# Optimization experiments

Measured on AMD Instinct MI355X. Metric: run time of the kernel, lower is better.

## Reference

```python
import jax, jax.numpy as jnp
import numpy as np

N = 4096        # number_of_users
IN = 1000       # in_size (items)
H1, H2 = 2048, 1024
EMB = 512
HEADS = 8
OUT = 1000


def setup_inputs() -> dict:
    key = jax.random.key(0)
    ks = iter(jax.random.split(key, 32))
    def lin(i, o):
        return jax.random.normal(next(ks), (i, o), jnp.float32) * (1.0 / np.sqrt(i))
    inp = {"batch": jax.random.normal(next(ks), (N, IN), jnp.float32)}
    for p in ("q", "k", "v"):
        inp[p + "_w1"] = lin(IN, H1); inp[p + "_b1"] = jnp.zeros((H1,), jnp.float32)
        inp[p + "_w2"] = lin(H1, H2); inp[p + "_b2"] = jnp.zeros((H2,), jnp.float32)
        inp[p + "_w3"] = lin(H2, EMB); inp[p + "_b3"] = jnp.zeros((EMB,), jnp.float32)
    inp["wo_w"] = lin(EMB, OUT)
    inp["wo_b"] = jnp.zeros((OUT,), jnp.float32)
    return inp


def _mlp(x, w1, b1, w2, b2, w3, b3):
    h = jax.nn.relu(x @ w1 + b1)
    h = jax.nn.relu(h @ w2 + b2)
    return h @ w3 + b3


def _split_heads(x):
    # [N, EMB] -> [HEADS, N, depth]
    return x.reshape(N, HEADS, EMB // HEADS).transpose(1, 0, 2)


def reference(batch,
              q_w1, q_b1, q_w2, q_b2, q_w3, q_b3,
              k_w1, k_b1, k_w2, k_b2, k_w3, k_b3,
              v_w1, v_b1, v_w2, v_b2, v_w3, v_b3,
              wo_w, wo_b):
    q = _mlp(batch, q_w1, q_b1, q_w2, q_b2, q_w3, q_b3)
    k = _mlp(batch, k_w1, k_b1, k_w2, k_b2, k_w3, k_b3)
    v = _mlp(batch, v_w1, v_b1, v_w2, v_b2, v_w3, v_b3)
    qh = jax.nn.relu(_split_heads(q))
    kh = jax.nn.relu(_split_heads(k))
    vh = _split_heads(v)
    depth = EMB // HEADS
    # ReLU-normalized attention (no softmax): scores / row-sum
    scores = jnp.einsum('hnd,hmd->hnm', qh, kh) / jnp.sqrt(jnp.float32(depth))
    denom = jnp.sum(scores, axis=-1, keepdims=True) + 1e-8
    weights = scores / denom
    att = jnp.einsum('hnm,hmd->hnd', weights, vh)   # [H, N, depth]
    att = att.transpose(1, 0, 2).reshape(N, EMB)
    return att @ wo_w + wo_b
```

## Files before the change

### kernel.cpp

```cpp
#include <hip/hip_runtime.h>
#include <hip/hip_bf16.h>


typedef __attribute__((ext_vector_type(4))) float f32x4;
typedef __attribute__((ext_vector_type(8))) short bf16x8;

static constexpr size_t OFF_XB   = 0;
static constexpr size_t OFF_WT1  = OFF_XB   + 8388608;
static constexpr size_t OFF_WT2  = OFF_WT1  + 12582912;
static constexpr size_t OFF_WT3  = OFF_WT2  + 12582912;
static constexpr size_t OFF_WTO  = OFF_WT3  + 3145728;
static constexpr size_t OFF_B1C  = OFF_WTO  + 1048576;
static constexpr size_t OFF_H1   = OFF_B1C  + 24576;
static constexpr size_t OFF_H2   = OFF_H1   + 50331648;
static constexpr size_t OFF_QKV  = OFF_H2   + 25165824;
static constexpr size_t OFF_MP   = OFF_QKV  + 12582912;
static constexpr size_t OFF_MF   = OFF_MP   + 4259840;
static constexpr size_t OFF_ATT  = OFF_MF   + 133120;

__device__ __forceinline__ void gload16(const __hip_bfloat16* g, __hip_bfloat16* l) {
  __builtin_amdgcn_global_load_lds(
      (const __attribute__((address_space(1))) void*)g,
      (__attribute__((address_space(3))) void*)l, 16, 0, 0);
}

__global__ void conv_pad_batch(const float* __restrict__ in, __hip_bfloat16* __restrict__ out) {
  int idx = blockIdx.x * 256 + threadIdx.x;
  int r = idx >> 10, c = idx & 1023;
  float v = (c < 1000) ? in[(size_t)r * 1000 + c] : 0.f;
  out[idx] = __float2bfloat16(v);
}

__global__ void concat3(const float* __restrict__ a, const float* __restrict__ b,
                        const float* __restrict__ c, float* __restrict__ out) {
  int i = blockIdx.x * 256 + threadIdx.x;
  if (i < 6144) {
    const float* src = (i < 2048) ? a : ((i < 4096) ? b : c);
    out[i] = src[i & 2047];
  }
}

__global__ void transpose_conv3(const float* __restrict__ s0, const float* __restrict__ s1,
                                const float* __restrict__ s2, __hip_bfloat16* __restrict__ outb,
                                size_t ostride, int K, int N, int Kpad) {
  const float* in = (blockIdx.z == 0) ? s0 : ((blockIdx.z == 1) ? s1 : s2);
  __hip_bfloat16* out = outb + (size_t)blockIdx.z * ostride;
  __shared__ float tile[32][33];
  int kb = blockIdx.x * 32, nb = blockIdx.y * 32;
  int tx = threadIdx.x, ty = threadIdx.y;
  for (int i = ty; i < 32; i += 8) {
    int k = kb + i, n = nb + tx;
    tile[i][tx] = (k < K && n < N) ? in[(size_t)k * N + n] : 0.f;
  }
  __syncthreads();
  for (int i = ty; i < 32; i += 8) {
    int n = nb + i, kp = kb + tx;
    out[(size_t)n * Kpad + kp] = __float2bfloat16(tile[tx][i]);
  }
}

__global__ __launch_bounds__(512, 2) void gemm_p8(
    const __hip_bfloat16* __restrict__ A, int lda, size_t Az,
    const __hip_bfloat16* __restrict__ B, int ldb, size_t Bz,
    const float* __restrict__ bias0, const float* __restrict__ bias1,
    const float* __restrict__ bias2,
    __hip_bfloat16* __restrict__ Cout, int ldc, size_t Cz,
    int NT, int relu) {
  __shared__ __hip_bfloat16 sm[2][4][8192];
  const int t = threadIdx.x;
  const int z = blockIdx.z;
  const int m0 = blockIdx.y * 256, n0 = blockIdx.x * 256;
  A += (size_t)z * Az;
  B += (size_t)z * Bz;
  const float* bias = (z == 0) ? bias0 : ((z == 1) ? bias1 : bias2);

  const int w = t >> 6, l = t & 63;
  const int wm = w >> 2, wn = w & 3;
  const int fr = l & 15, fq = l >> 4;

  const int row0 = t >> 3, row1 = row0 + 64;
  const int c0 = (t & 7) ^ (row0 & 7);
  const int c1 = (t & 7) ^ (row1 & 7);
  const __hip_bfloat16* gA0a = A + (size_t)(m0 + row0) * lda + c0 * 8;
  const __hip_bfloat16* gA0b = A + (size_t)(m0 + row1) * lda + c1 * 8;
  const __hip_bfloat16* gA1a = gA0a + (size_t)128 * lda;
  const __hip_bfloat16* gA1b = gA0b + (size_t)128 * lda;
  const __hip_bfloat16* gB0a = B + (size_t)(n0 + row0) * ldb + c0 * 8;
  const __hip_bfloat16* gB0b = B + (size_t)(n0 + row1) * ldb + c1 * 8;
  const __hip_bfloat16* gB1a = gB0a + (size_t)128 * ldb;
  const __hip_bfloat16* gB1b = gB0b + (size_t)128 * ldb;

  const int baseA = (wm * 64 + fr) * 128;
  const int baseB = (wn * 32 + fr) * 128;
  const int xb0 = ((fq) ^ (fr & 7)) * 16;
  const int xb1 = ((4 + fq) ^ (fr & 7)) * 16;

  f32x4 acc[8][4] = {};
  bf16x8 af[4][2], bfv[2][2];

#define STG8(NXT, HALF, PA, PB, KT) do {                                       \
    gload16((PA) + (size_t)(KT) * 64, &sm[NXT][HALF][w * 512]);                \
    gload16((PB) + (size_t)(KT) * 64, &sm[NXT][HALF][w * 512 + 4096]);         \
  } while (0)

#define PH8(CUR, MG, NG, RDA, RDB, STG, WAITSTMT) do {                         \
    const char* a_ = (const char*)&sm[CUR][MG][0];                             \
    const char* b_ = (const char*)&sm[CUR][2 + (NG)][0];                       \
    if (RDA) {                                                                 \
      _Pragma("unroll") for (int i = 0; i < 4; ++i) {                          \
        af[i][0] = *(const bf16x8*)(a_ + baseA + i * 2048 + xb0);              \
        af[i][1] = *(const bf16x8*)(a_ + baseA + i * 2048 + xb1);              \
      }                                                                        \
    }                                                                          \
    if (RDB) {                                                                 \
      _Pragma("unroll") for (int j = 0; j < 2; ++j) {                          \
        bfv[j][0] = *(const bf16x8*)(b_ + baseB + j * 2048 + xb0);             \
        bfv[j][1] = *(const bf16x8*)(b_ + baseB + j * 2048 + xb1);             \
      }                                                                        \
    }                                                                          \
    STG;                                                                       \
    __builtin_amdgcn_s_barrier();                                              \
    asm volatile("s_waitcnt lgkmcnt(0)" ::: "memory");                         \
    __builtin_amdgcn_sched_barrier(0);                                         \
    __builtin_amdgcn_s_setprio(1);                                             \
    _Pragma("unroll") for (int ks = 0; ks < 2; ++ks)                           \
      _Pragma("unroll") for (int i = 0; i < 4; ++i)                            \
        _Pragma("unroll") for (int j = 0; j < 2; ++j)                          \
          acc[(MG) * 4 + i][(NG) * 2 + j] =                                    \
              __builtin_amdgcn_mfma_f32_16x16x32_bf16(                         \
                  af[i][ks], bfv[j][ks], acc[(MG) * 4 + i][(NG) * 2 + j],      \
                  0, 0, 0);                                                    \
    __builtin_amdgcn_s_setprio(0);                                             \
    WAITSTMT;                                                                  \
    __builtin_amdgcn_s_barrier();                                              \
  } while (0)

  STG8(0, 0, gA0a, gA0b, 0);
  STG8(0, 1, gA1a, gA1b, 0);
  STG8(0, 2, gB0a, gB0b, 0);
  STG8(0, 3, gB1a, gB1b, 0);
  asm volatile("s_waitcnt vmcnt(0)" ::: "memory");
  __builtin_amdgcn_s_barrier();

  for (int T = 0; T < NT - 1; ++T) {
    const int cur = T & 1, nxt = cur ^ 1;
    const int kt = T + 1;
    PH8(cur, 0, 0, 1, 1, STG8(nxt, 0, gA0a, gA0b, kt), (void)0);
    PH8(cur, 1, 0, 1, 0, STG8(nxt, 1, gA1a, gA1b, kt),
        asm volatile("s_waitcnt vmcnt(4)" ::: "memory"));
    PH8(cur, 1, 1, 0, 1, STG8(nxt, 2, gB0a, gB0b, kt), (void)0);
    PH8(cur, 0, 1, 1, 0, STG8(nxt, 3, gB1a, gB1b, kt),
        asm volatile("s_waitcnt vmcnt(2)" ::: "memory"));
  }
  {
    const int cur = (NT - 1) & 1;
    PH8(cur, 0, 0, 1, 1, (void)0, (void)0);
    PH8(cur, 1, 0, 1, 0, (void)0,
        asm volatile("s_waitcnt vmcnt(0)" ::: "memory"));
    PH8(cur, 1, 1, 0, 1, (void)0, (void)0);
    PH8(cur, 0, 1, 1, 0, (void)0, (void)0);
  }
#undef PH8
#undef STG8

  __hip_bfloat16* C = Cout + (size_t)z * Cz;
  float bv[4];
#pragma unroll
  for (int nj = 0; nj < 4; ++nj) {
    const int col = n0 + (nj >> 1) * 128 + wn * 32 + (nj & 1) * 16 + fr;
    bv[nj] = bias[col];
  }
#pragma unroll
  for (int mi = 0; mi < 8; ++mi) {
    const int rowb = m0 + (mi >> 2) * 128 + wm * 64 + (mi & 3) * 16 + fq * 4;
#pragma unroll
    for (int nj = 0; nj < 4; ++nj) {
      const int col = n0 + (nj >> 1) * 128 + wn * 32 + (nj & 1) * 16 + fr;
#pragma unroll
      for (int rr = 0; rr < 4; ++rr) {
        float v = acc[mi][nj][rr] + bv[nj];
        if (relu) v = fmaxf(v, 0.f);
        C[(size_t)(rowb + rr) * ldc + col] = __float2bfloat16(v);
      }
    }
  }
}

__global__ __launch_bounds__(256) void gemm_bt(
    const __hip_bfloat16* __restrict__ A, int lda, size_t Az,
    const __hip_bfloat16* __restrict__ B, int ldb, size_t Bz,
    const float* __restrict__ bias0, const float* __restrict__ bias1,
    const float* __restrict__ bias2,
    void* __restrict__ Cout, int ldc, size_t Cz,
    int nlimit, int K, int epi) {
  __shared__ __hip_bfloat16 As[128 * 32];
  __shared__ __hip_bfloat16 Bs[128 * 32];
  const int t = threadIdx.x;
  const int z = blockIdx.z;
  const int m0 = blockIdx.y * 128;
  const int n0 = blockIdx.x * 128;
  A += (size_t)z * Az;
  B += (size_t)z * Bz;
  const float* bias = (z == 0) ? bias0 : ((z == 1) ? bias1 : bias2);
  const int w = t >> 6, l = t & 63;
  const int wm = (w >> 1) * 64, wn = (w & 1) * 64;
  const int fr = l & 15, fq = l >> 4;
  const int sr = t >> 2, sc = (t & 3) * 8;

  f32x4 acc[4][4] = {};

  const __hip_bfloat16* ga = A + (size_t)(m0 + sr) * lda + sc;
  const __hip_bfloat16* gb = B + (size_t)(n0 + sr) * ldb + sc;
  __hip_bfloat16* la = As + w * 512;
  __hip_bfloat16* lb = Bs + w * 512;

  for (int k0 = 0; k0 < K; k0 += 32) {
    gload16(ga, la);
    gload16(ga + (size_t)64 * lda, la + 2048);
    gload16(gb, lb);
    gload16(gb + (size_t)64 * ldb, lb + 2048);
    ga += 32; gb += 32;
    __syncthreads();
    bf16x8 af[4], bfr[4];
#pragma unroll
    for (int i = 0; i < 4; ++i) {
      af[i]  = *reinterpret_cast<const bf16x8*>(&As[(wm + i * 16 + fr) * 32 + fq * 8]);
      bfr[i] = *reinterpret_cast<const bf16x8*>(&Bs[(wn + i * 16 + fr) * 32 + fq * 8]);
    }
#pragma unroll
    for (int i = 0; i < 4; ++i)
#pragma unroll
      for (int j = 0; j < 4; ++j)
        acc[i][j] = __builtin_amdgcn_mfma_f32_16x16x32_bf16(af[i], bfr[j], acc[i][j], 0, 0, 0);
    __syncthreads();
  }

  const bool dorelu = (epi == 1) || (epi == 3 && z < 2);
  float bv[4];
#pragma unroll
  for (int j = 0; j < 4; ++j) {
    int col = n0 + wn + j * 16 + fr;
    bv[j] = (col < nlimit) ? bias[col] : 0.f;
  }
#pragma unroll
  for (int i = 0; i < 4; ++i) {
#pragma unroll
    for (int j = 0; j < 4; ++j) {
      int col = n0 + wn + j * 16 + fr;
#pragma unroll
      for (int r = 0; r < 4; ++r) {
        int row = m0 + wm + i * 16 + fq * 4 + r;
        float v = acc[i][j][r] + bv[j];
        if (dorelu) v = fmaxf(v, 0.f);
        if (epi == 2) {
          if (col < nlimit)
            ((float*)Cout)[(size_t)row * ldc + col] = v;
        } else {
          ((__hip_bfloat16*)Cout + (size_t)z * Cz)[(size_t)row * ldc + col] = __float2bfloat16(v);
        }
      }
    }
  }
}

__global__ __launch_bounds__(256) void kv_outer(const __hip_bfloat16* __restrict__ QKV, int ld,
                                                float* __restrict__ part) {
  __shared__ __hip_bfloat16 kt[128][64];
  __shared__ __hip_bfloat16 vt[128][64];
  const int t = threadIdx.x;
  const int n0 = blockIdx.x * 128;
  const int h = blockIdx.y;
#pragma unroll
  for (int it = 0; it < 4; ++it) {
    int r = it * 32 + (t >> 3);
    int c = (t & 7) * 8;
    const __hip_bfloat16* kr = &QKV[(size_t)(n0 + r) * ld + 512 + h * 64 + c];
    const __hip_bfloat16* vr = &QKV[(size_t)(n0 + r) * ld + 1024 + h * 64 + c];
    *reinterpret_cast<bf16x8*>(&kt[r][c]) = *reinterpret_cast<const bf16x8*>(kr);
    *reinterpret_cast<bf16x8*>(&vt[r][c]) = *reinterpret_cast<const bf16x8*>(vr);
  }
  __syncthreads();
  const int i = t >> 2, j0 = (t & 3) << 4;
  float acc[16] = {};
  float ks = 0.f;
  for (int r = 0; r < 128; ++r) {
    float kv = __bfloat162float(kt[r][i]);
    ks += kv;
#pragma unroll
    for (int jj = 0; jj < 16; ++jj)
      acc[jj] += kv * __bfloat162float(vt[r][j0 + jj]);
  }
  float* dst = part + ((size_t)blockIdx.x * 8 + h) * 4160;
#pragma unroll
  for (int jj = 0; jj < 16; ++jj) dst[i * 64 + j0 + jj] = acc[jj];
  if ((t & 3) == 0) dst[4096 + i] = ks;
}

__global__ void reduce_m(const float* __restrict__ part, float* __restrict__ Mfin) {
  int h = blockIdx.x, t = threadIdx.x;
  for (int idx = t; idx < 4160; idx += 256) {
    float s = 0.f;
    for (int c = 0; c < 32; ++c) s += part[((size_t)c * 8 + h) * 4160 + idx];
    Mfin[(size_t)h * 4160 + idx] = s;
  }
}

__global__ __launch_bounds__(256) void att_kernel(const __hip_bfloat16* __restrict__ QKV, int ld,
                                                  const float* __restrict__ Mfin,
                                                  __hip_bfloat16* __restrict__ att) {
  __shared__ float q[8][512];
  __shared__ float den[8][8];
  const int t = threadIdx.x;
  const int n0 = blockIdx.x * 8;
  for (int e = t; e < 8 * 512; e += 256) {
    int r = e >> 9, c = e & 511;
    q[r][c] = __bfloat162float(QKV[(size_t)(n0 + r) * ld + c]);
  }
  __syncthreads();
  if (t < 64) {
    int r = t >> 3, h = t & 7;
    const float* ks = Mfin + (size_t)h * 4160 + 4096;
    float s = 0.f;
    for (int i = 0; i < 64; ++i) s += q[r][h * 64 + i] * ks[i];
    den[r][h] = s * 0.125f + 1e-8f;
  }
  __syncthreads();
  for (int cc = 0; cc < 2; ++cc) {
    int j = t + cc * 256;
    int h = j >> 6, jh = j & 63;
    const float* Mc = Mfin + (size_t)h * 4160;
    float a0[8] = {};
    for (int i = 0; i < 64; ++i) {
      float m = Mc[i * 64 + jh];
#pragma unroll
      for (int r = 0; r < 8; ++r) a0[r] += q[r][h * 64 + i] * m;
    }
#pragma unroll
    for (int r = 0; r < 8; ++r)
      att[(size_t)(n0 + r) * 512 + j] = __float2bfloat16(a0[r] * 0.125f / den[r][h]);
  }
}

extern "C" void kernel_launch(void* const* d_in, const int* in_sizes, int n_in,
                              void* d_out, int out_size, void* d_ws, size_t ws_size,
                              hipStream_t stream) {
  const float* batch = (const float*)d_in[0];
  const float* w1[3] = {(const float*)d_in[1],  (const float*)d_in[7],  (const float*)d_in[13]};
  const float* b1[3] = {(const float*)d_in[2],  (const float*)d_in[8],  (const float*)d_in[14]};
  const float* w2[3] = {(const float*)d_in[3],  (const float*)d_in[9],  (const float*)d_in[15]};
  const float* b2[3] = {(const float*)d_in[4],  (const float*)d_in[10], (const float*)d_in[16]};
  const float* w3[3] = {(const float*)d_in[5],  (const float*)d_in[11], (const float*)d_in[17]};
  const float* b3[3] = {(const float*)d_in[6],  (const float*)d_in[12], (const float*)d_in[18]};
  const float* wow   = (const float*)d_in[19];
  const float* wob   = (const float*)d_in[20];

  char* ws = (char*)d_ws;
  __hip_bfloat16* XB  = (__hip_bfloat16*)(ws + OFF_XB);
  __hip_bfloat16* WT1 = (__hip_bfloat16*)(ws + OFF_WT1);
  __hip_bfloat16* WT2 = (__hip_bfloat16*)(ws + OFF_WT2);
  __hip_bfloat16* WT3 = (__hip_bfloat16*)(ws + OFF_WT3);
  __hip_bfloat16* WTO = (__hip_bfloat16*)(ws + OFF_WTO);
  float*          B1C = (float*)(ws + OFF_B1C);
  __hip_bfloat16* H1  = (__hip_bfloat16*)(ws + OFF_H1);
  __hip_bfloat16* H2  = (__hip_bfloat16*)(ws + OFF_H2);
  __hip_bfloat16* QKV = (__hip_bfloat16*)(ws + OFF_QKV);
  float*          MP  = (float*)(ws + OFF_MP);
  float*          MF  = (float*)(ws + OFF_MF);
  __hip_bfloat16* ATT = (__hip_bfloat16*)(ws + OFF_ATT);
  float*          OUT = (float*)d_out;

  conv_pad_batch<<<16384, 256, 0, stream>>>(batch, XB);
  concat3<<<24, 256, 0, stream>>>(b1[0], b1[1], b1[2], B1C);
  transpose_conv3<<<dim3(32, 64, 3), dim3(32, 8), 0, stream>>>(
      w1[0], w1[1], w1[2], WT1, (size_t)2048 * 1024, 1000, 2048, 1024);
  transpose_conv3<<<dim3(64, 32, 3), dim3(32, 8), 0, stream>>>(
      w2[0], w2[1], w2[2], WT2, (size_t)1024 * 2048, 2048, 1024, 2048);
  transpose_conv3<<<dim3(32, 16, 3), dim3(32, 8), 0, stream>>>(
      w3[0], w3[1], w3[2], WT3, (size_t)512 * 1024, 1024, 512, 1024);
  transpose_conv3<<<dim3(16, 32, 1), dim3(32, 8), 0, stream>>>(
      wow, wow, wow, WTO, 0, 512, 1000, 512);

  gemm_p8<<<dim3(24, 16, 1), 512, 0, stream>>>(XB, 1024, 0, WT1, 1024, 0,
                                               B1C, B1C, B1C, H1, 6144, 0, 16, 1);
  gemm_p8<<<dim3(4, 16, 3), 512, 0, stream>>>(H1, 6144, 2048, WT2, 2048, (size_t)1024 * 2048,
                                              b2[0], b2[1], b2[2], H2, 3072, 1024, 32, 1);
  gemm_bt<<<dim3(4, 32, 3), 256, 0, stream>>>(H2, 3072, 1024, WT3, 1024, (size_t)512 * 1024,
                                              b3[0], b3[1], b3[2], QKV, 1536, 512,
                                              512, 1024, 3);

  kv_outer<<<dim3(32, 8), 256, 0, stream>>>(QKV, 1536, MP);
  reduce_m<<<8, 256, 0, stream>>>(MP, MF);
  att_kernel<<<512, 256, 0, stream>>>(QKV, 1536, MF, ATT);

  gemm_bt<<<dim3(8, 32, 1), 256, 0, stream>>>(ATT, 512, 0, WTO, 512, 0,
                                              wob, wob, wob, OUT, 1000, 0,
                                              1000, 512, 2);

  (void)in_sizes; (void)n_in; (void)out_size; (void)ws_size;
}
```

Before: 282.7 us.

## Fold attention M into output weights, add XCD block swizzle, reorder LDS reads

Precomputes M·Wo per head (mw_kernel) so the final GEMM consumes a per-row scaled Q directly. This replaces the attention kernel, the Wo transpose and the separate att-times-Wo path with a tiny kernel and a cheap qscale kernel. Adds an XCD-aware block index swizzle to both GEMMs to improve L2 locality. It also reorders LDS fragment reads and drops the explicit lgkmcnt wait, which relies on the compiler inserting the needed waits. mw_kernel is serial per thread, 64x64 MACs over only 128 blocks, so it could be slow.

Result: slower. 435.6 us (+54.1%).

```diff
diff --git a/kernel.cpp b/kernel.cpp
--- a/kernel.cpp
+++ b/kernel.cpp
@@ -9,19 +9,26 @@
 static constexpr size_t OFF_WT1  = OFF_XB   + 8388608;
 static constexpr size_t OFF_WT2  = OFF_WT1  + 12582912;
 static constexpr size_t OFF_WT3  = OFF_WT2  + 12582912;
-static constexpr size_t OFF_WTO  = OFF_WT3  + 3145728;
-static constexpr size_t OFF_B1C  = OFF_WTO  + 1048576;
+static constexpr size_t OFF_MWT  = OFF_WT3  + 3145728;
+static constexpr size_t OFF_B1C  = OFF_MWT  + 1048576;
 static constexpr size_t OFF_H1   = OFF_B1C  + 24576;
 static constexpr size_t OFF_H2   = OFF_H1   + 50331648;
 static constexpr size_t OFF_QKV  = OFF_H2   + 25165824;
 static constexpr size_t OFF_MP   = OFF_QKV  + 12582912;
 static constexpr size_t OFF_MF   = OFF_MP   + 4259840;
-static constexpr size_t OFF_ATT  = OFF_MF   + 133120;
+static constexpr size_t OFF_QT   = OFF_MF   + 133120;
 
 __device__ __forceinline__ void gload16(const __hip_bfloat16* g, __hip_bfloat16* l) {
   __builtin_amdgcn_global_load_lds(
       (const __attribute__((address_space(1))) void*)g,
       (__attribute__((address_space(3))) void*)l, 16, 0, 0);
+}
+
+__device__ __forceinline__ int xcd_swz(int orig, int nwg) {
+  const int qq = nwg >> 3, rr = nwg & 7;
+  const int xcd = orig & 7, off = orig >> 3;
+  return (xcd < rr) ? (xcd * (qq + 1) + off)
+                    : (rr * (qq + 1) + (xcd - rr) * qq + off);
 }
 
 __global__ void conv_pad_batch(const float* __restrict__ in, __hip_bfloat16* __restrict__ out) {
@@ -69,7 +76,9 @@
   __shared__ __hip_bfloat16 sm[2][4][8192];
   const int t = threadIdx.x;
   const int z = blockIdx.z;
-  const int m0 = blockIdx.y * 256, n0 = blockIdx.x * 256;
+  const int gx = gridDim.x;
+  const int id2 = xcd_swz(blockIdx.y * gx + blockIdx.x, gx * gridDim.y);
+  const int m0 = (id2 / gx) * 256, n0 = (id2 % gx) * 256;
   A += (size_t)z * Az;
   B += (size_t)z * Bz;
   const float* bias = (z == 0) ? bias0 : ((z == 1) ? bias1 : bias2);
@@ -107,20 +116,23 @@
     const char* a_ = (const char*)&sm[CUR][MG][0];                             \
     const char* b_ = (const char*)&sm[CUR][2 + (NG)][0];                       \
     if (RDA) {                                                                 \
-      _Pragma("unroll") for (int i = 0; i < 4; ++i) {                          \
+      _Pragma("unroll") for (int i = 0; i < 4; ++i)                            \
         af[i][0] = *(const bf16x8*)(a_ + baseA + i * 2048 + xb0);              \
-        af[i][1] = *(const bf16x8*)(a_ + baseA + i * 2048 + xb1);              \
-      }                                                                        \
     }                                                                          \
     if (RDB) {                                                                 \
-      _Pragma("unroll") for (int j = 0; j < 2; ++j) {                          \
+      _Pragma("unroll") for (int j = 0; j < 2; ++j)                            \
         bfv[j][0] = *(const bf16x8*)(b_ + baseB + j * 2048 + xb0);             \
+    }                                                                          \
+    if (RDA) {                                                                 \
+      _Pragma("unroll") for (int i = 0; i < 4; ++i)                            \
+        af[i][1] = *(const bf16x8*)(a_ + baseA + i * 2048 + xb1);              \
+    }                                                                          \
+    if (RDB) {                                                                 \
+      _Pragma("unroll") for (int j = 0; j < 2; ++j)                            \
         bfv[j][1] = *(const bf16x8*)(b_ + baseB + j * 2048 + xb1);             \
-      }                                                                        \
     }                                                                          \
     STG;                                                                       \
     __builtin_amdgcn_s_barrier();                                              \
-    asm volatile("s_waitcnt lgkmcnt(0)" ::: "memory");                         \
     __builtin_amdgcn_sched_barrier(0);                                         \
     __builtin_amdgcn_s_setprio(1);                                             \
     _Pragma("unroll") for (int ks = 0; ks < 2; ++ks)                           \
@@ -197,8 +209,9 @@
   __shared__ __hip_bfloat16 Bs[128 * 32];
   const int t = threadIdx.x;
   const int z = blockIdx.z;
-  const int m0 = blockIdx.y * 128;
-  const int n0 = blockIdx.x * 128;
+  const int gx = gridDim.x;
+  const int id2 = xcd_swz(blockIdx.y * gx + blockIdx.x, gx * gridDim.y);
+  const int m0 = (id2 / gx) * 128, n0 = (id2 % gx) * 128;
   A += (size_t)z * Az;
   B += (size_t)z * Bz;
   const float* bias = (z == 0) ? bias0 : ((z == 1) ? bias1 : bias2);
@@ -305,40 +318,51 @@
   }
 }
 
-__global__ __launch_bounds__(256) void att_kernel(const __hip_bfloat16* __restrict__ QKV, int ld,
-                                                  const float* __restrict__ Mfin,
-                                                  __hip_bfloat16* __restrict__ att) {
-  __shared__ float q[8][512];
-  __shared__ float den[8][8];
+__global__ void mw_kernel(const float* __restrict__ Mfin, const float* __restrict__ wo,
+                          __hip_bfloat16* __restrict__ MWT) {
+  const int h = blockIdx.y;
+  const int j = blockIdx.x * 64 + threadIdx.x;
+  const float* M = Mfin + (size_t)h * 4160;
+  if (j < 1000) {
+    for (int i = 0; i < 64; ++i) {
+      float a = 0.f;
+      for (int d = 0; d < 64; ++d)
+        a += M[i * 64 + d] * wo[(size_t)(h * 64 + d) * 1000 + j];
+      MWT[(size_t)j * 512 + h * 64 + i] = __float2bfloat16(a);
+    }
+  } else {
+    for (int i = 0; i < 64; ++i)
+      MWT[(size_t)j * 512 + h * 64 + i] = __float2bfloat16(0.f);
+  }
+}
+
+__global__ __launch_bounds__(256) void qscale(const __hip_bfloat16* __restrict__ QKV,
+                                              const float* __restrict__ Mfin,
+                                              __hip_bfloat16* __restrict__ QT) {
   const int t = threadIdx.x;
-  const int n0 = blockIdx.x * 8;
-  for (int e = t; e < 8 * 512; e += 256) {
-    int r = e >> 9, c = e & 511;
-    q[r][c] = __bfloat162float(QKV[(size_t)(n0 + r) * ld + c]);
-  }
-  __syncthreads();
-  if (t < 64) {
-    int r = t >> 3, h = t & 7;
-    const float* ks = Mfin + (size_t)h * 4160 + 4096;
-    float s = 0.f;
-    for (int i = 0; i < 64; ++i) s += q[r][h * 64 + i] * ks[i];
-    den[r][h] = s * 0.125f + 1e-8f;
-  }
-  __syncthreads();
-  for (int cc = 0; cc < 2; ++cc) {
-    int j = t + cc * 256;
-    int h = j >> 6, jh = j & 63;
-    const float* Mc = Mfin + (size_t)h * 4160;
-    float a0[8] = {};
-    for (int i = 0; i < 64; ++i) {
-      float m = Mc[i * 64 + jh];
-#pragma unroll
-      for (int r = 0; r < 8; ++r) a0[r] += q[r][h * 64 + i] * m;
-    }
-#pragma unroll
-    for (int r = 0; r < 8; ++r)
-      att[(size_t)(n0 + r) * 512 + j] = __float2bfloat16(a0[r] * 0.125f / den[r][h]);
-  }
+  const int r = blockIdx.x * 4 + (t >> 6);
+  const int c = (t & 63) * 8;
+  const int h = (t & 63) >> 3;
+  bf16x8 qv = *reinterpret_cast<const bf16x8*>(&QKV[(size_t)r * 1536 + c]);
+  float qf[8];
+#pragma unroll
+  for (int j = 0; j < 8; ++j)
+    qf[j] = __bfloat162float(*(const __hip_bfloat16*)&((const short*)&qv)[j]);
+  const float* ks = Mfin + (size_t)h * 4160 + 4096 + (c & 63);
+  float s = 0.f;
+#pragma unroll
+  for (int j = 0; j < 8; ++j) s += qf[j] * ks[j];
+  s += __shfl_xor(s, 1, 8);
+  s += __shfl_xor(s, 2, 8);
+  s += __shfl_xor(s, 4, 8);
+  const float inv = 0.125f / (s * 0.125f + 1e-8f);
+  bf16x8 o;
+#pragma unroll
+  for (int j = 0; j < 8; ++j) {
+    __hip_bfloat16 b = __float2bfloat16(qf[j] * inv);
+    ((short*)&o)[j] = *(const short*)&b;
+  }
+  *reinterpret_cast<bf16x8*>(&QT[(size_t)r * 512 + c]) = o;
 }
 
 extern "C" void kernel_launch(void* const* d_in, const int* in_sizes, int n_in,
@@ -359,14 +383,14 @@
   __hip_bfloat16* WT1 = (__hip_bfloat16*)(ws + OFF_WT1);
   __hip_bfloat16* WT2 = (__hip_bfloat16*)(ws + OFF_WT2);
   __hip_bfloat16* WT3 = (__hip_bfloat16*)(ws + OFF_WT3);
-  __hip_bfloat16* WTO = (__hip_bfloat16*)(ws + OFF_WTO);
+  __hip_bfloat16* MWT = (__hip_bfloat16*)(ws + OFF_MWT);
   float*          B1C = (float*)(ws + OFF_B1C);
   __hip_bfloat16* H1  = (__hip_bfloat16*)(ws + OFF_H1);
   __hip_bfloat16* H2  = (__hip_bfloat16*)(ws + OFF_H2);
   __hip_bfloat16* QKV = (__hip_bfloat16*)(ws + OFF_QKV);
   float*          MP  = (float*)(ws + OFF_MP);
   float*          MF  = (float*)(ws + OFF_MF);
-  __hip_bfloat16* ATT = (__hip_bfloat16*)(ws + OFF_ATT);
+  __hip_bfloat16* QT  = (__hip_bfloat16*)(ws + OFF_QT);
   float*          OUT = (float*)d_out;
 
   conv_pad_batch<<<16384, 256, 0, stream>>>(batch, XB);
@@ -377,8 +401,6 @@
       w2[0], w2[1], w2[2], WT2, (size_t)1024 * 2048, 2048, 1024, 2048);
   transpose_conv3<<<dim3(32, 16, 3), dim3(32, 8), 0, stream>>>(
       w3[0], w3[1], w3[2], WT3, (size_t)512 * 1024, 1024, 512, 1024);
-  transpose_conv3<<<dim3(16, 32, 1), dim3(32, 8), 0, stream>>>(
-      wow, wow, wow, WTO, 0, 512, 1000, 512);
 
   gemm_p8<<<dim3(24, 16, 1), 512, 0, stream>>>(XB, 1024, 0, WT1, 1024, 0,
                                                B1C, B1C, B1C, H1, 6144, 0, 16, 1);
@@ -390,9 +412,10 @@
 
   kv_outer<<<dim3(32, 8), 256, 0, stream>>>(QKV, 1536, MP);
   reduce_m<<<8, 256, 0, stream>>>(MP, MF);
-  att_kernel<<<512, 256, 0, stream>>>(QKV, 1536, MF, ATT);
-
-  gemm_bt<<<dim3(8, 32, 1), 256, 0, stream>>>(ATT, 512, 0, WTO, 512, 0,
+  mw_kernel<<<dim3(16, 8), 64, 0, stream>>>(MF, wow, MWT);
+  qscale<<<1024, 256, 0, stream>>>(QKV, MF, QT);
+
+  gemm_bt<<<dim3(8, 32, 1), 256, 0, stream>>>(QT, 512, 0, MWT, 512, 0,
                                               wob, wob, wob, OUT, 1000, 0,
                                               1000, 512, 2);
 
```
